# Kernel tuning notes

Measured on AMD Instinct MI355X. Metric: run time of the kernel, lower is better.

Reference implementation:

```python
import jax, jax.numpy as jnp
import numpy as np

B = 8192
E = 1024  # embedding_size
P = 512   # projection_size
TEMPERATURE = 0.1
NEG_INF = -9e15
EPS = 1e-8


def setup_inputs() -> dict:
    key = jax.random.key(0)
    kx, kw, kb = jax.random.split(key, 3)
    x = jax.random.normal(kx, (B, 2 * E), dtype=jnp.float32)
    lim = 1.0 / np.sqrt(E)
    # torch nn.Linear default init: uniform(-1/sqrt(in), 1/sqrt(in))
    w = jax.random.uniform(kw, (E, P), jnp.float32, -lim, lim)
    b = jax.random.uniform(kb, (P,), jnp.float32, -lim, lim)
    return {"x": x, "w": w, "b": b}


def reference(x, w, b):
    e = x.shape[1] // 2
    # NOTE: source applies codon_projection to BOTH halves (aminoacid_projection unused)
    z_codon = jax.nn.relu(x[:, :e]) @ w + b          # [B, P]
    z_amino = jax.nn.relu(x[:, e:]) @ w + b          # [B, P]
    z = jnp.concatenate([z_codon, z_amino], axis=1)  # [B, 2P]

    # cosine similarity via normalize + GEMM instead of O(B^2*D) broadcast
    norm = jnp.maximum(jnp.linalg.norm(z, axis=-1, keepdims=True), EPS)
    zn = z / norm
    cos_sim = zn @ zn.T                              # [B, B]

    n = cos_sim.shape[0]
    idx = jnp.arange(n)
    # mask self-similarity BEFORE temperature division (matches source order)
    cos_sim = jnp.where(idx[:, None] == idx[None, :], NEG_INF, cos_sim)
    cos_sim = cos_sim / TEMPERATURE

    # pos_mask = eye rolled by B//2 along dim 0: pos[i] = cos_sim[i, (i - B//2) % B]
    pos = cos_sim[idx, (idx - n // 2) % n]
    nll = -pos + jax.nn.logsumexp(cos_sim, axis=-1)
    return nll.mean()
```

## Files before the change

### kernel.cpp

```cpp
#include <hip/hip_runtime.h>
#include <hip/hip_bf16.h>
#include <stdint.h>


typedef __attribute__((ext_vector_type(8))) __bf16 bf16x8;
typedef __attribute__((ext_vector_type(4))) float f32x4;
typedef __attribute__((ext_vector_type(4))) int i32x4;
typedef __attribute__((ext_vector_type(8))) int i32x8;

__device__ __forceinline__ unsigned short f2bf(float f) {
  union { float f; unsigned int u; } v; v.f = f;
  unsigned int u = v.u;
  u += 0x7FFFu + ((u >> 16) & 1u);
  return (unsigned short)(u >> 16);
}

__device__ __forceinline__ float bf2f(unsigned short s) {
  return __uint_as_float(((unsigned int)s) << 16);
}

__global__ __launch_bounds__(256) void prep2_kernel(
    const float* __restrict__ x, const float* __restrict__ w,
    unsigned char* __restrict__ x8, unsigned char* __restrict__ wt8,
    float* __restrict__ sumexp, float* __restrict__ out) {
  int tid = blockIdx.x * 256 + threadIdx.x;
  float4 v = ((const float4*)x)[tid];
  int p = __builtin_amdgcn_cvt_pk_fp8_f32(fmaxf(v.x, 0.f) * 16.f,
                                          fmaxf(v.y, 0.f) * 16.f, 0, false);
  p = __builtin_amdgcn_cvt_pk_fp8_f32(fmaxf(v.z, 0.f) * 16.f,
                                      fmaxf(v.w, 0.f) * 16.f, p, true);
  ((int*)x8)[tid] = p;
  if (tid < 512 * 1024) {
    int k = tid & 1023, n = tid >> 10;
    int q = __builtin_amdgcn_cvt_pk_fp8_f32(w[k * 512 + n] * 64.f, 0.f, 0, false);
    wt8[(n << 10) + k] = (unsigned char)(q & 0xFF);
  }
  if (tid < 8192) sumexp[tid] = 0.f;
  if (tid == 0) out[0] = 0.f;
}

__global__ __launch_bounds__(256) void gemm1q_kernel(
    const unsigned char* __restrict__ x8, const unsigned char* __restrict__ wt8,
    const float* __restrict__ bias, unsigned short* __restrict__ z) {
  __shared__ unsigned char As[16384] __attribute__((aligned(16)));
  __shared__ unsigned char Bs[16384] __attribute__((aligned(16)));
  int b = blockIdx.x;
  int kk = b >> 3;
  int i0 = ((b & 7) * 16 + (kk >> 2)) * 128;
  int n0 = (kk & 3) * 128;

  int tid = threadIdx.x, L = tid & 63, w = tid >> 6;
  int wm = w >> 1, wn = w & 1;
  int l4 = L & 15, q = L >> 4;
  int panel = q * 4096;

  int lp = L ^ ((L >> 3) & 7);
  int srow = w * 32 + (lp >> 1), sh = lp & 1;

  f32x4 acc[4][4];
#pragma unroll
  for (int a = 0; a < 4; ++a)
#pragma unroll
    for (int bq = 0; bq < 4; ++bq) acc[a][bq] = (f32x4)0.f;

  const unsigned char* Ag = x8 + (size_t)(i0 + srow) * 1024 + sh * 16;
  const unsigned char* Bg = wt8 + (size_t)(n0 + srow) * 1024 + sh * 16;

#pragma unroll 1
  for (int k0 = 0; k0 < 1024; k0 += 128) {
    __syncthreads();
#pragma unroll
    for (int t = 0; t < 4; ++t)
      __builtin_amdgcn_global_load_lds(
          (const __attribute__((address_space(1))) void*)(Ag + k0 + t * 32),
          (__attribute__((address_space(3))) void*)(As + t * 4096 + (tid & ~63) * 16),
          16, 0, 0);
#pragma unroll
    for (int t = 0; t < 4; ++t)
      __builtin_amdgcn_global_load_lds(
          (const __attribute__((address_space(1))) void*)(Bg + k0 + t * 32),
          (__attribute__((address_space(3))) void*)(Bs + t * 4096 + (tid & ~63) * 16),
          16, 0, 0);
    __syncthreads();
    i32x8 afr[4];
#pragma unroll
    for (int mt = 0; mt < 4; ++mt) {
      int row = wm * 64 + mt * 16 + l4;
      int p0 = (row * 2) ^ ((row >> 2) & 7);
      i32x4 lo = *(const i32x4*)(As + panel + p0 * 16);
      i32x4 hi = *(const i32x4*)(As + panel + (p0 ^ 1) * 16);
      afr[mt] = (i32x8){lo.x, lo.y, lo.z, lo.w, hi.x, hi.y, hi.z, hi.w};
    }
#pragma unroll
    for (int nt = 0; nt < 4; ++nt) {
      int row = wn * 64 + nt * 16 + l4;
      int p0 = (row * 2) ^ ((row >> 2) & 7);
      i32x4 lo = *(const i32x4*)(Bs + panel + p0 * 16);
      i32x4 hi = *(const i32x4*)(Bs + panel + (p0 ^ 1) * 16);
      i32x8 bfr = (i32x8){lo.x, lo.y, lo.z, lo.w, hi.x, hi.y, hi.z, hi.w};
#pragma unroll
      for (int mt = 0; mt < 4; ++mt)
        acc[mt][nt] = __builtin_amdgcn_mfma_scale_f32_16x16x128_f8f6f4(
            afr[mt], bfr, acc[mt][nt], 0, 0,
            0, 0x7F7F7F7F, 0, 0x7F7F7F7F);
    }
  }

  const float SC = 1.0f / 1024.0f;
#pragma unroll
  for (int nt = 0; nt < 4; ++nt) {
    int n = n0 + wn * 64 + nt * 16 + l4;
    float bn = bias[n];
#pragma unroll
    for (int mt = 0; mt < 4; ++mt) {
      int ib = i0 + wm * 64 + mt * 16 + q * 4;
#pragma unroll
      for (int r = 0; r < 4; ++r)
        z[(size_t)(ib + r) * 512 + n] = f2bf(acc[mt][nt][r] * SC + bn);
    }
  }
}

__global__ __launch_bounds__(256) void norm_kernel(
    const unsigned short* __restrict__ z, unsigned char* __restrict__ zn8) {
  int row = blockIdx.x, t = threadIdx.x;
  ushort4 u = ((const ushort4*)z)[row * 256 + t];
  float a0 = bf2f(u.x), a1 = bf2f(u.y), a2 = bf2f(u.z), a3 = bf2f(u.w);
  float ss = a0 * a0 + a1 * a1 + a2 * a2 + a3 * a3;
#pragma unroll
  for (int off = 1; off < 64; off <<= 1) ss += __shfl_xor(ss, off);
  __shared__ float red[4];
  if ((t & 63) == 0) red[t >> 6] = ss;
  __syncthreads();
  float tot = red[0] + red[1] + red[2] + red[3];
  float inv = 16.f / fmaxf(sqrtf(tot), 1e-8f);
  int p = __builtin_amdgcn_cvt_pk_fp8_f32(a0 * inv, a1 * inv, 0, false);
  p = __builtin_amdgcn_cvt_pk_fp8_f32(a2 * inv, a3 * inv, p, true);
  ((int*)zn8)[row * 256 + t] = p;
}

__global__ __launch_bounds__(256, 3) void gemm2_kernel(
    const unsigned char* __restrict__ zn8,
    float* __restrict__ sumexp, float* __restrict__ pos) {
  __shared__ unsigned char As[16384] __attribute__((aligned(16)));
  __shared__ unsigned char Bs[16384] __attribute__((aligned(16)));
  int g = (blockIdx.x & 7) * 260 + (blockIdx.x >> 3);
  int SI = 0, rem = g;
#pragma unroll 1
  for (SI = 0; SI < 8; ++SI) {
    int rowcnt = 36 + (7 - SI) * 64;
    if (rem < rowcnt) break;
    rem -= rowcnt;
  }
  int bi, bj;
  if (rem < 36) {
    int ti = 0;
    while (rem >= 8 - ti) { rem -= 8 - ti; ++ti; }
    bi = SI * 8 + ti;
    bj = bi + rem;
  } else {
    rem -= 36;
    int SJ = SI + 1 + (rem >> 6);
    int l = rem & 63;
    bi = SI * 8 + (l >> 3);
    bj = SJ * 8 + (l & 7);
  }
  bool diag = (bi == bj);
  int i0 = bi * 128, j0 = bj * 128;

  int tid = threadIdx.x, L = tid & 63, w = tid >> 6;
  int wm = w >> 1, wn = w & 1;
  int l4 = L & 15;
  int panel = (L >> 4) * 4096;

  int lp = L ^ ((L >> 3) & 7);
  int srow = w * 32 + (lp >> 1), sh = lp & 1;

  f32x4 acc[4][4];
#pragma unroll
  for (int a = 0; a < 4; ++a)
#pragma unroll
    for (int bq = 0; bq < 4; ++bq) acc[a][bq] = (f32x4)0.f;

  const unsigned char* Ag = zn8 + (i0 + srow) * 1024 + sh * 16;
  const unsigned char* Bg = zn8 + (j0 + srow) * 1024 + sh * 16;
  const unsigned char* Bsrc = diag ? (const unsigned char*)As : (const unsigned char*)Bs;

#pragma unroll 1
  for (int k0 = 0; k0 < 1024; k0 += 128) {
    __syncthreads();
#pragma unroll
    for (int t = 0; t < 4; ++t)
      __builtin_amdgcn_global_load_lds(
          (const __attribute__((address_space(1))) void*)(Ag + k0 + t * 32),
          (__attribute__((address_space(3))) void*)(As + t * 4096 + (tid & ~63) * 16),
          16, 0, 0);
    if (!diag) {
#pragma unroll
      for (int t = 0; t < 4; ++t)
        __builtin_amdgcn_global_load_lds(
            (const __attribute__((address_space(1))) void*)(Bg + k0 + t * 32),
            (__attribute__((address_space(3))) void*)(Bs + t * 4096 + (tid & ~63) * 16),
            16, 0, 0);
    }
    __syncthreads();
    i32x8 afr[4];
#pragma unroll
    for (int mt = 0; mt < 4; ++mt) {
      int row = wm * 64 + mt * 16 + l4;
      int p0 = (row * 2) ^ ((row >> 2) & 7);
      i32x4 lo = *(const i32x4*)(As + panel + p0 * 16);
      i32x4 hi = *(const i32x4*)(As + panel + (p0 ^ 1) * 16);
      afr[mt] = (i32x8){lo.x, lo.y, lo.z, lo.w, hi.x, hi.y, hi.z, hi.w};
    }
#pragma unroll
    for (int nt = 0; nt < 4; ++nt) {
      int row = wn * 64 + nt * 16 + l4;
      int p0 = (row * 2) ^ ((row >> 2) & 7);
      i32x4 lo = *(const i32x4*)(Bsrc + panel + p0 * 16);
      i32x4 hi = *(const i32x4*)(Bsrc + panel + (p0 ^ 1) * 16);
      i32x8 bfr = (i32x8){lo.x, lo.y, lo.z, lo.w, hi.x, hi.y, hi.z, hi.w};
#pragma unroll
      for (int mt = 0; mt < 4; ++mt)
        acc[mt][nt] = __builtin_amdgcn_mfma_scale_f32_16x16x128_f8f6f4(
            afr[mt], bfr, acc[mt][nt], 0, 0,
            0, 0x7F7F7F7F, 0, 0x7F7F7F7F);
    }
  }

  const float SC = 10.0f / 256.0f;
  float rs[4][4];
  float cs[4] = {0.f, 0.f, 0.f, 0.f};
#pragma unroll
  for (int mt = 0; mt < 4; ++mt)
#pragma unroll
    for (int r = 0; r < 4; ++r) rs[mt][r] = 0.f;
  int ib = i0 + wm * 64 + ((L >> 4) << 2);
  int jb = j0 + wn * 64 + l4;
#pragma unroll
  for (int mt = 0; mt < 4; ++mt)
#pragma unroll
    for (int nt = 0; nt < 4; ++nt) {
      int j = jb + nt * 16;
#pragma unroll
      for (int r = 0; r < 4; ++r) {
        int i = ib + mt * 16 + r;
        float s = acc[mt][nt][r] * SC;
        if (j == (i ^ 4096)) { pos[i] = s; pos[j] = s; }
        float e = (i == j) ? 0.f : __expf(s);
        rs[mt][r] += e;
        if (!diag) cs[nt] += e;
      }
    }
#pragma unroll
  for (int mt = 0; mt < 4; ++mt)
#pragma unroll
    for (int r = 0; r < 4; ++r) {
      float v = rs[mt][r];
      v += __shfl_xor(v, 1); v += __shfl_xor(v, 2);
      v += __shfl_xor(v, 4); v += __shfl_xor(v, 8);
      rs[mt][r] = v;
    }
  int sel = l4;
  float myv = rs[0][0];
#pragma unroll
  for (int mt = 0; mt < 4; ++mt)
#pragma unroll
    for (int r = 0; r < 4; ++r)
      if (sel == mt * 4 + r) myv = rs[mt][r];
  int rowi = i0 + wm * 64 + (sel >> 2) * 16 + ((L >> 4) << 2) + (sel & 3);
  atomicAdd(&sumexp[rowi], myv);
  if (!diag) {
#pragma unroll
    for (int nt = 0; nt < 4; ++nt) {
      float v = cs[nt];
      v += __shfl_xor(v, 16); v += __shfl_xor(v, 32);
      if ((L >> 4) == 0) atomicAdd(&sumexp[jb + nt * 16], v);
    }
  }
}

__global__ __launch_bounds__(512) void finalize_kernel(
    const float* __restrict__ sumexp, const float* __restrict__ pos,
    float* __restrict__ out) {
  int t = threadIdx.x;
  int i = blockIdx.x * 512 + t;
  float s = logf(sumexp[i]) - pos[i];
#pragma unroll
  for (int off = 1; off < 64; off <<= 1) s += __shfl_xor(s, off);
  __shared__ float red[8];
  if ((t & 63) == 0) red[t >> 6] = s;
  __syncthreads();
  if (t == 0) {
    float tot = 0.f;
    for (int k2 = 0; k2 < 8; ++k2) tot += red[k2];
    atomicAdd(out, tot * (1.0f / 8192.0f));
  }
}

extern "C" void kernel_launch(void* const* d_in, const int* in_sizes, int n_in,
                              void* d_out, int out_size, void* d_ws, size_t ws_size,
                              hipStream_t stream) {
  const float* x = (const float*)d_in[0];
  const float* w = (const float*)d_in[1];
  const float* b = (const float*)d_in[2];
  float* out = (float*)d_out;
  char* ws = (char*)d_ws;
  unsigned char* wt8 = (unsigned char*)(ws);
  unsigned char* x8  = (unsigned char*)(ws + 1048576);
  unsigned short* z  = (unsigned short*)(ws + 17825792);
  unsigned char* zn8 = (unsigned char*)(ws + 68157440);
  float* sumexp      = (float*)(ws + 84934656);
  float* pos         = (float*)(ws + 84967424);

  prep2_kernel<<<16384, 256, 0, stream>>>(x, w, x8, wt8, sumexp, out);
  gemm1q_kernel<<<512, 256, 0, stream>>>(x8, wt8, b, z);
  norm_kernel<<<8192, 256, 0, stream>>>(z, zn8);
  gemm2_kernel<<<2080, 256, 0, stream>>>(zn8, sumexp, pos);
  finalize_kernel<<<16, 512, 0, stream>>>(sumexp, pos, out);
}
```

Measured before the change: 175.4 us.

## Fuse row normalization into projection GEMM and transpose weights via LDS tile

Folds the L2 row-normalization and fp8 quantization into the first GEMM epilogue, so the bf16 z intermediate and the separate norm kernel are gone. The GEMM is restructured so each 512-thread block owns 64 full rows across all 512 output columns, with double-buffered LDS staging that overlaps loads with MFMA work. Weight transpose/quantization moves out of the x-conversion kernel into a dedicated tiled LDS transpose kernel that reads coalesced. The trade-offs are a very large LDS footprint (~144KB) limiting occupancy, and byte-wise scattered fp8 stores in the epilogue.

```diff
diff --git a/kernel.cpp b/kernel.cpp
--- a/kernel.cpp
+++ b/kernel.cpp
@@ -3,25 +3,17 @@
 #include <stdint.h>
 
 
-typedef __attribute__((ext_vector_type(8))) __bf16 bf16x8;
 typedef __attribute__((ext_vector_type(4))) float f32x4;
 typedef __attribute__((ext_vector_type(4))) int i32x4;
 typedef __attribute__((ext_vector_type(8))) int i32x8;
 
-__device__ __forceinline__ unsigned short f2bf(float f) {
-  union { float f; unsigned int u; } v; v.f = f;
-  unsigned int u = v.u;
-  u += 0x7FFFu + ((u >> 16) & 1u);
-  return (unsigned short)(u >> 16);
-}
-
-__device__ __forceinline__ float bf2f(unsigned short s) {
-  return __uint_as_float(((unsigned int)s) << 16);
+__device__ __forceinline__ unsigned char f2fp8(float f) {
+  int q = __builtin_amdgcn_cvt_pk_fp8_f32(f, 0.f, 0, false);
+  return (unsigned char)(q & 0xFF);
 }
 
 __global__ __launch_bounds__(256) void prep2_kernel(
-    const float* __restrict__ x, const float* __restrict__ w,
-    unsigned char* __restrict__ x8, unsigned char* __restrict__ wt8,
+    const float* __restrict__ x, unsigned char* __restrict__ x8,
     float* __restrict__ sumexp, float* __restrict__ out) {
   int tid = blockIdx.x * 256 + threadIdx.x;
   float4 v = ((const float4*)x)[tid];
@@ -30,32 +22,78 @@
   p = __builtin_amdgcn_cvt_pk_fp8_f32(fmaxf(v.z, 0.f) * 16.f,
                                       fmaxf(v.w, 0.f) * 16.f, p, true);
   ((int*)x8)[tid] = p;
-  if (tid < 512 * 1024) {
-    int k = tid & 1023, n = tid >> 10;
-    int q = __builtin_amdgcn_cvt_pk_fp8_f32(w[k * 512 + n] * 64.f, 0.f, 0, false);
-    wt8[(n << 10) + k] = (unsigned char)(q & 0xFF);
-  }
   if (tid < 8192) sumexp[tid] = 0.f;
   if (tid == 0) out[0] = 0.f;
 }
 
-__global__ __launch_bounds__(256) void gemm1q_kernel(
+__global__ __launch_bounds__(256) void wtr_kernel(
+    const float* __restrict__ w, unsigned char* __restrict__ wt8) {
+  __shared__ unsigned char lt[64][68];
+  int b = blockIdx.x, t = threadIdx.x;
+  int k0 = (b >> 3) * 64, n0 = (b & 7) * 64;
+  int r = t >> 4, c = t & 15;
+#pragma unroll
+  for (int i = 0; i < 4; ++i) {
+    int kl = i * 16 + r;
+    float4 v = *(const float4*)&w[(size_t)(k0 + kl) * 512 + n0 + c * 4];
+    int q = __builtin_amdgcn_cvt_pk_fp8_f32(v.x * 64.f, v.y * 64.f, 0, false);
+    q = __builtin_amdgcn_cvt_pk_fp8_f32(v.z * 64.f, v.w * 64.f, q, true);
+    *(int*)&lt[kl][c * 4] = q;
+  }
+  __syncthreads();
+  int nl = t >> 2, ks = t & 3;
+  union { unsigned char b8[16]; i32x4 v4; } u;
+#pragma unroll
+  for (int j = 0; j < 16; ++j) u.b8[j] = lt[ks * 16 + j][nl];
+  *(i32x4*)&wt8[(size_t)(n0 + nl) * 1024 + k0 + ks * 16] = u.v4;
+}
+
+__global__ __launch_bounds__(512, 2) void gemm1qn_kernel(
     const unsigned char* __restrict__ x8, const unsigned char* __restrict__ wt8,
-    const float* __restrict__ bias, unsigned short* __restrict__ z) {
-  __shared__ unsigned char As[16384] __attribute__((aligned(16)));
-  __shared__ unsigned char Bs[16384] __attribute__((aligned(16)));
-  int b = blockIdx.x;
-  int kk = b >> 3;
-  int i0 = ((b & 7) * 16 + (kk >> 2)) * 128;
-  int n0 = (kk & 3) * 128;
-
+    const float* __restrict__ bias, unsigned char* __restrict__ zn8) {
+  __shared__ unsigned char smem[147456] __attribute__((aligned(16)));
+  int i0 = blockIdx.x * 64;
   int tid = threadIdx.x, L = tid & 63, w = tid >> 6;
-  int wm = w >> 1, wn = w & 1;
   int l4 = L & 15, q = L >> 4;
-  int panel = q * 4096;
-
-  int lp = L ^ ((L >> 3) & 7);
-  int srow = w * 32 + (lp >> 1), sh = lp & 1;
+
+  int sA = tid & 127, pA = tid >> 7;
+  int eA = sA ^ ((sA >> 3) & 7);
+  int rA = eA >> 1, hA = eA & 1;
+  const unsigned char* srcA = x8 + (size_t)(i0 + rA) * 1024 + pA * 32 + hA * 16;
+  int e1 = tid ^ ((tid >> 3) & 7);
+  int rB = e1 >> 1, hB = e1 & 1;
+  const unsigned char* srcB1 = wt8 + (size_t)rB * 1024 + hB * 16;
+  const unsigned char* srcB2 = wt8 + (size_t)(rB + 256) * 1024 + hB * 16;
+
+  auto stage = [&](int buf, int k0) {
+    __builtin_amdgcn_global_load_lds(
+        (const __attribute__((address_space(1))) void*)(srcA + k0),
+        (__attribute__((address_space(3))) void*)(smem + buf * 8192 + tid * 16),
+        16, 0, 0);
+#pragma unroll
+    for (int p = 0; p < 4; ++p) {
+      __builtin_amdgcn_global_load_lds(
+          (const __attribute__((address_space(1))) void*)(srcB1 + k0 + p * 32),
+          (__attribute__((address_space(3))) void*)(smem + 16384 + buf * 65536 + p * 16384 + tid * 16),
+          16, 0, 0);
+      __builtin_amdgcn_global_load_lds(
+          (const __attribute__((address_space(1))) void*)(srcB2 + k0 + p * 32),
+          (__attribute__((address_space(3))) void*)(smem + 16384 + buf * 65536 + p * 16384 + 8192 + tid * 16),
+          16, 0, 0);
+    }
+  };
+
+  int pAo[4], pBo[4];
+#pragma unroll
+  for (int mt = 0; mt < 4; ++mt) {
+    int r = mt * 16 + l4;
+    pAo[mt] = ((r * 2) ^ ((r >> 2) & 7)) * 16;
+  }
+#pragma unroll
+  for (int nt = 0; nt < 4; ++nt) {
+    int r = w * 64 + nt * 16 + l4;
+    pBo[nt] = ((r * 2) ^ ((r >> 2) & 7)) * 16;
+  }
 
   f32x4 acc[4][4];
 #pragma unroll
@@ -63,40 +101,24 @@
 #pragma unroll
     for (int bq = 0; bq < 4; ++bq) acc[a][bq] = (f32x4)0.f;
 
-  const unsigned char* Ag = x8 + (size_t)(i0 + srow) * 1024 + sh * 16;
-  const unsigned char* Bg = wt8 + (size_t)(n0 + srow) * 1024 + sh * 16;
-
+  stage(0, 0);
+  __syncthreads();
 #pragma unroll 1
-  for (int k0 = 0; k0 < 1024; k0 += 128) {
-    __syncthreads();
-#pragma unroll
-    for (int t = 0; t < 4; ++t)
-      __builtin_amdgcn_global_load_lds(
-          (const __attribute__((address_space(1))) void*)(Ag + k0 + t * 32),
-          (__attribute__((address_space(3))) void*)(As + t * 4096 + (tid & ~63) * 16),
-          16, 0, 0);
-#pragma unroll
-    for (int t = 0; t < 4; ++t)
-      __builtin_amdgcn_global_load_lds(
-          (const __attribute__((address_space(1))) void*)(Bg + k0 + t * 32),
-          (__attribute__((address_space(3))) void*)(Bs + t * 4096 + (tid & ~63) * 16),
-          16, 0, 0);
-    __syncthreads();
+  for (int s = 0; s < 8; ++s) {
+    if (s < 7) stage((s + 1) & 1, (s + 1) * 128);
+    const unsigned char* Ab = smem + (s & 1) * 8192 + q * 2048;
+    const unsigned char* Bb = smem + 16384 + (s & 1) * 65536 + q * 16384;
     i32x8 afr[4];
 #pragma unroll
     for (int mt = 0; mt < 4; ++mt) {
-      int row = wm * 64 + mt * 16 + l4;
-      int p0 = (row * 2) ^ ((row >> 2) & 7);
-      i32x4 lo = *(const i32x4*)(As + panel + p0 * 16);
-      i32x4 hi = *(const i32x4*)(As + panel + (p0 ^ 1) * 16);
+      i32x4 lo = *(const i32x4*)(Ab + pAo[mt]);
+      i32x4 hi = *(const i32x4*)(Ab + (pAo[mt] ^ 16));
       afr[mt] = (i32x8){lo.x, lo.y, lo.z, lo.w, hi.x, hi.y, hi.z, hi.w};
     }
 #pragma unroll
     for (int nt = 0; nt < 4; ++nt) {
-      int row = wn * 64 + nt * 16 + l4;
-      int p0 = (row * 2) ^ ((row >> 2) & 7);
-      i32x4 lo = *(const i32x4*)(Bs + panel + p0 * 16);
-      i32x4 hi = *(const i32x4*)(Bs + panel + (p0 ^ 1) * 16);
+      i32x4 lo = *(const i32x4*)(Bb + pBo[nt]);
+      i32x4 hi = *(const i32x4*)(Bb + (pBo[nt] ^ 16));
       i32x8 bfr = (i32x8){lo.x, lo.y, lo.z, lo.w, hi.x, hi.y, hi.z, hi.w};
 #pragma unroll
       for (int mt = 0; mt < 4; ++mt)
@@ -104,39 +126,67 @@
             afr[mt], bfr, acc[mt][nt], 0, 0,
             0, 0x7F7F7F7F, 0, 0x7F7F7F7F);
     }
+    __syncthreads();
   }
 
   const float SC = 1.0f / 1024.0f;
-#pragma unroll
-  for (int nt = 0; nt < 4; ++nt) {
-    int n = n0 + wn * 64 + nt * 16 + l4;
-    float bn = bias[n];
-#pragma unroll
-    for (int mt = 0; mt < 4; ++mt) {
-      int ib = i0 + wm * 64 + mt * 16 + q * 4;
+  float bn[4];
+#pragma unroll
+  for (int nt = 0; nt < 4; ++nt) bn[nt] = bias[w * 64 + nt * 16 + l4];
+  float ssp[4][4];
+#pragma unroll
+  for (int mt = 0; mt < 4; ++mt)
+#pragma unroll
+    for (int r = 0; r < 4; ++r) ssp[mt][r] = 0.f;
+#pragma unroll
+  for (int mt = 0; mt < 4; ++mt)
+#pragma unroll
+    for (int nt = 0; nt < 4; ++nt)
+#pragma unroll
+      for (int r = 0; r < 4; ++r) {
+        float zv = acc[mt][nt][r] * SC + bn[nt];
+        acc[mt][nt][r] = zv;
+        ssp[mt][r] += zv * zv;
+      }
+#pragma unroll
+  for (int mt = 0; mt < 4; ++mt)
+#pragma unroll
+    for (int r = 0; r < 4; ++r) {
+      float v = ssp[mt][r];
+      v += __shfl_xor(v, 1); v += __shfl_xor(v, 2);
+      v += __shfl_xor(v, 4); v += __shfl_xor(v, 8);
+      ssp[mt][r] = v;
+    }
+  float* ssbuf = (float*)smem;
+  if (l4 == 0) {
+#pragma unroll
+    for (int mt = 0; mt < 4; ++mt)
 #pragma unroll
       for (int r = 0; r < 4; ++r)
-        z[(size_t)(ib + r) * 512 + n] = f2bf(acc[mt][nt][r] * SC + bn);
-    }
-  }
-}
-
-__global__ __launch_bounds__(256) void norm_kernel(
-    const unsigned short* __restrict__ z, unsigned char* __restrict__ zn8) {
-  int row = blockIdx.x, t = threadIdx.x;
-  ushort4 u = ((const ushort4*)z)[row * 256 + t];
-  float a0 = bf2f(u.x), a1 = bf2f(u.y), a2 = bf2f(u.z), a3 = bf2f(u.w);
-  float ss = a0 * a0 + a1 * a1 + a2 * a2 + a3 * a3;
-#pragma unroll
-  for (int off = 1; off < 64; off <<= 1) ss += __shfl_xor(ss, off);
-  __shared__ float red[4];
-  if ((t & 63) == 0) red[t >> 6] = ss;
-  __syncthreads();
-  float tot = red[0] + red[1] + red[2] + red[3];
-  float inv = 16.f / fmaxf(sqrtf(tot), 1e-8f);
-  int p = __builtin_amdgcn_cvt_pk_fp8_f32(a0 * inv, a1 * inv, 0, false);
-  p = __builtin_amdgcn_cvt_pk_fp8_f32(a2 * inv, a3 * inv, p, true);
-  ((int*)zn8)[row * 256 + t] = p;
+        ssbuf[(mt * 16 + q * 4 + r) * 8 + w] = ssp[mt][r];
+  }
+  __syncthreads();
+  float* invbuf = (float*)(smem + 2048);
+  if (tid < 32) {
+    float tot = 0.f;
+#pragma unroll
+    for (int j = 0; j < 8; ++j)
+      tot += ssbuf[(2 * tid) * 8 + j] + ssbuf[(2 * tid + 1) * 8 + j];
+    invbuf[tid] = 16.f / fmaxf(sqrtf(tot), 1e-8f);
+  }
+  __syncthreads();
+#pragma unroll
+  for (int mt = 0; mt < 4; ++mt)
+#pragma unroll
+    for (int r = 0; r < 4; ++r) {
+      int zr = mt * 16 + q * 4 + r;
+      float inv = invbuf[zr >> 1];
+      int zg = i0 + zr;
+      size_t base = (size_t)(zg >> 1) * 1024 + (zg & 1) * 512 + w * 64 + l4;
+#pragma unroll
+      for (int nt = 0; nt < 4; ++nt)
+        zn8[base + nt * 16] = f2fp8(acc[mt][nt][r] * inv);
+    }
 }
 
 __global__ __launch_bounds__(256, 3) void gemm2_kernel(
@@ -308,14 +358,13 @@
   char* ws = (char*)d_ws;
   unsigned char* wt8 = (unsigned char*)(ws);
   unsigned char* x8  = (unsigned char*)(ws + 1048576);
-  unsigned short* z  = (unsigned short*)(ws + 17825792);
   unsigned char* zn8 = (unsigned char*)(ws + 68157440);
   float* sumexp      = (float*)(ws + 84934656);
   float* pos         = (float*)(ws + 84967424);
 
-  prep2_kernel<<<16384, 256, 0, stream>>>(x, w, x8, wt8, sumexp, out);
-  gemm1q_kernel<<<512, 256, 0, stream>>>(x8, wt8, b, z);
-  norm_kernel<<<8192, 256, 0, stream>>>(z, zn8);
+  prep2_kernel<<<16384, 256, 0, stream>>>(x, x8, sumexp, out);
+  wtr_kernel<<<128, 256, 0, stream>>>(w, wt8);
+  gemm1qn_kernel<<<256, 512, 0, stream>>>(x8, wt8, b, zn8);
   gemm2_kernel<<<2080, 256, 0, stream>>>(zn8, sumexp, pos);
   finalize_kernel<<<16, 512, 0, stream>>>(sumexp, pos, out);
 }
```

Measured after the change: 175.8 us. About the same (+0.2%).
